# Kernel optimization log

Hardware: AMD Instinct MI355X
Metric: run time of the kernel (lower is better)

## Reference

```python
import jax, jax.numpy as jnp
import numpy as np

B, C, H, W, K = 4, 64, 128, 128, 3
K2 = K * K
PAD = (K - 1) // 2  # same padding for 3x3


def setup_inputs() -> dict:
    key = jax.random.key(0)
    ks = jax.random.split(key, 9)
    s = 0.05
    return {
        "x": jax.random.normal(ks[0], (B, C, H, W), jnp.float32),
        "inter": jax.random.normal(ks[1], (B, C, H, W), jnp.float32),
        # offset/mask predictor conv: input cat([x, inter]) -> 3*K2 channels (dy, dx, mask)
        "w_offset": jax.random.normal(ks[2], (3 * K2, 2 * C, K, K), jnp.float32) * s,
        "b_offset": jnp.zeros((3 * K2,), jnp.float32),
        # deformable conv weight (bias=False per DGM init)
        "w_dcn": jax.random.normal(ks[3], (C, C, K, K), jnp.float32) * s,
        # SFT gamma branch: two 1x1 convs (bias=False)
        "w_g1": jax.random.normal(ks[4], (C, C), jnp.float32) * s,
        "w_g2": jax.random.normal(ks[5], (C, C), jnp.float32) * s,
        # SFT beta branch: two 1x1 convs (bias=False)
        "w_b1": jax.random.normal(ks[6], (C, C), jnp.float32) * s,
        "w_b2": jax.random.normal(ks[7], (C, C), jnp.float32) * s,
    }


def _lrelu(v):
    # LeakyReLU(0.1)
    return jnp.where(v >= 0, v, 0.1 * v)


def _conv(x, w, b=None):
    y = jax.lax.conv_general_dilated(
        x, w, window_strides=(1, 1), padding=[(PAD, PAD), (PAD, PAD)],
        dimension_numbers=("NCHW", "OIHW", "NCHW"))
    if b is not None:
        y = y + b[None, :, None, None]
    return y


def _bilinear_gather(x, py, px):
    """x: [B,C,H,W]; py, px: [B,K2,H,W] float sample coords.
    Returns samples [B,K2,H,W,C]; out-of-bounds treated as zero (DCN zero-pad)."""
    y0 = jnp.floor(py)
    x0 = jnp.floor(px)
    wy = (py - y0)[..., None]
    wx = (px - x0)[..., None]

    def gather(yi, xi):
        valid = ((yi >= 0) & (yi < H) & (xi >= 0) & (xi < W)).astype(x.dtype)
        yc = jnp.clip(yi, 0, H - 1).astype(jnp.int32)
        xc = jnp.clip(xi, 0, W - 1).astype(jnp.int32)
        bidx = jnp.arange(B)[:, None, None, None]
        v = x[bidx, :, yc, xc]  # advanced indexing -> [B,K2,H,W,C]
        return v * valid[..., None]

    v00 = gather(y0, x0)
    v01 = gather(y0, x0 + 1)
    v10 = gather(y0 + 1, x0)
    v11 = gather(y0 + 1, x0 + 1)
    return (v00 * (1 - wy) * (1 - wx) + v01 * (1 - wy) * wx
            + v10 * wy * (1 - wx) + v11 * wy * wx)


def _dgm_forward(x, inter, w_offset, b_offset, w_dcn, w_g1, w_g2, w_b1, w_b2):
    # --- WADCN branch: modulated deformable conv, offsets predicted from cat(x, inter)
    om = _conv(jnp.concatenate([x, inter], axis=1), w_offset, b_offset)  # [B,3K2,H,W]
    dy, dx, m = jnp.split(om, 3, axis=1)  # each [B,K2,H,W]
    mask = jax.nn.sigmoid(m)

    ky, kx = jnp.meshgrid(jnp.arange(K), jnp.arange(K), indexing="ij")
    ky = ky.reshape(K2).astype(x.dtype)
    kx = kx.reshape(K2).astype(x.dtype)
    hh = jnp.arange(H, dtype=x.dtype)
    ww = jnp.arange(W, dtype=x.dtype)
    # sample coords: base grid + kernel-tap offset + learned offset
    py = hh[None, None, :, None] + (ky - PAD)[None, :, None, None] + dy  # [B,K2,H,W]
    px = ww[None, None, None, :] + (kx - PAD)[None, :, None, None] + dx

    samp = _bilinear_gather(x, py, px) * mask[..., None]  # [B,K2,H,W,C]
    dcn_out = jnp.einsum("bkhwc,ock->bohw", samp, w_dcn.reshape(C, C, K2))

    # --- SFT branch: two 1x1-conv + LeakyReLU chains producing gamma/beta
    gamma = jnp.einsum("oc,bchw->bohw", w_g2,
                       _lrelu(jnp.einsum("oc,bchw->bohw", w_g1, inter)))
    beta = jnp.einsum("oc,bchw->bohw", w_b2,
                      _lrelu(jnp.einsum("oc,bchw->bohw", w_b1, inter)))
    sft_out = x * gamma + beta

    # --- fused residual combine (DGM.relu is defined but never applied)
    return x + dcn_out + sft_out


def reference(x, inter, w_offset, b_offset, w_dcn, w_g1, w_g2, w_b1, w_b2):
    return _dgm_forward(x, inter, w_offset, b_offset, w_dcn, w_g1, w_g2, w_b1, w_b2)
```

## Files before the change

kernel.cpp:

```cpp
#include <hip/hip_runtime.h>
#include <hip/hip_bf16.h>
#include <math.h>

#define BB 4
#define CC 64
#define HH 128
#define WW 128
#define HW (HH*WW)
#define NPIX (BB*HW)

typedef __attribute__((ext_vector_type(8))) short short8;
typedef __attribute__((ext_vector_type(4))) float f32x4;

__device__ __forceinline__ float bf2f(ushort u) {
  union { unsigned u; float f; } v; v.u = ((unsigned)u) << 16; return v.f;
}
__device__ __forceinline__ ushort f2bf(float f) {
  __hip_bfloat16 h = __float2bfloat16(f); return *(ushort*)&h;
}

__global__ __launch_bounds__(256) void k_transp(
    const float* __restrict__ x, const float* __restrict__ inter,
    ushort* __restrict__ x_clh, ushort* __restrict__ inter_clh) {
  __shared__ float tile[64 * 129];
  int blk = blockIdx.x;
  int sel = blk >> 9;
  int bh = blk & 511;
  int b = bh >> 7, h = bh & 127;
  const float* src = sel ? inter : x;
  ushort* dst = sel ? inter_clh : x_clh;
  const float* sp = src + (size_t)(b * 64) * HW + h * WW;
  for (int i = threadIdx.x; i < 64 * 128; i += 256) {
    int c = i >> 7, w = i & 127;
    tile[c * 129 + w] = sp[(size_t)c * HW + w];
  }
  __syncthreads();
  ushort* dp = dst + ((size_t)b * HW + h * WW) * 64;
  for (int i = threadIdx.x; i < 64 * 128; i += 256) {
    int w = i >> 6, c = i & 63;
    dp[w * 64 + c] = f2bf(tile[c * 129 + w]);
  }
}

__global__ void k_wprep(const float* __restrict__ w_off,
                        const float* __restrict__ w_dcn,
                        const float* __restrict__ wg1, const float* __restrict__ wb1,
                        const float* __restrict__ wg2, const float* __restrict__ wb2,
                        ushort* __restrict__ wfb, ushort* __restrict__ wdT,
                        ushort* __restrict__ w1gb, ushort* __restrict__ w1bb,
                        ushort* __restrict__ w2gb, ushort* __restrict__ w2bb,
                        float* __restrict__ zp) {
  int blk = blockIdx.x;
  if (blk < 144) {
    int i = blk * 256 + threadIdx.x;
    if (i < 64) zp[i] = 0.f;
    if (i < 9 * 32 * 128) {
      int tap = i >> 12, rem = i & 4095, m = rem >> 7, c = rem & 127;
      float v = (m < 27) ? w_off[(size_t)(m * 128 + c) * 9 + tap] : 0.f;
      wfb[i] = f2bf(v);
    }
  } else if (blk < 288) {
    int i = (blk - 144) * 256 + threadIdx.x;
    if (i < 64 * 64 * 9) {
      int o = i / 576, rem = i % 576, k = rem >> 6, c = rem & 63;
      wdT[i] = f2bf(w_dcn[(o * 64 + c) * 9 + k]);
    }
  } else {
    int i = (blk - 288) * 256 + threadIdx.x;
    int m = i >> 12, j = i & 4095;
    const float* src = (m == 0) ? wg1 : (m == 1) ? wb1 : (m == 2) ? wg2 : wb2;
    ushort* dst = (m == 0) ? w1gb : (m == 1) ? w1bb : (m == 2) ? w2gb : w2bb;
    dst[j] = f2bf(src[j]);
  }
}

#define FPITCH 72

__global__ __launch_bounds__(256) void k_sft(
    const float* __restrict__ x, const ushort* __restrict__ inter_clh,
    const ushort* __restrict__ w1gb, const ushort* __restrict__ w1bb,
    const ushort* __restrict__ w2gb, const ushort* __restrict__ w2bb,
    float* __restrict__ out) {
  __shared__ ushort Sg[64 * FPITCH];
  __shared__ ushort Sb[64 * FPITCH];
  int tid = threadIdx.x;
  int lane = tid & 63;
  int quad = lane >> 4, col = lane & 15;
  int pg0 = blockIdx.x * 64;
  int b = pg0 >> 14, hw0 = pg0 & 16383;
  int o_base = __builtin_amdgcn_readfirstlane((tid >> 6) * 16);

  f32x4 ag[4], ab[4];
#pragma unroll
  for (int nt = 0; nt < 4; ++nt) {
    ag[nt] = (f32x4){0.f, 0.f, 0.f, 0.f};
    ab[nt] = (f32x4){0.f, 0.f, 0.f, 0.f};
  }
#pragma unroll
  for (int ks = 0; ks < 2; ++ks) {
    short8 a_g = *(const short8*)(w1gb + (size_t)(o_base + col) * 64 + ks * 32 + quad * 8);
    short8 a_b = *(const short8*)(w1bb + (size_t)(o_base + col) * 64 + ks * 32 + quad * 8);
#pragma unroll
    for (int nt = 0; nt < 4; ++nt) {
      short8 bf = *(const short8*)(inter_clh + (size_t)(pg0 + nt * 16 + col) * 64 + ks * 32 + quad * 8);
      ag[nt] = __builtin_amdgcn_mfma_f32_16x16x32_bf16(a_g, bf, ag[nt], 0, 0, 0);
      ab[nt] = __builtin_amdgcn_mfma_f32_16x16x32_bf16(a_b, bf, ab[nt], 0, 0, 0);
    }
  }
#pragma unroll
  for (int nt = 0; nt < 4; ++nt) {
    int px = nt * 16 + col;
    ushort pkg[4], pkb[4];
#pragma unroll
    for (int r = 0; r < 4; ++r) {
      float vg = ag[nt][r]; vg = vg >= 0.f ? vg : 0.1f * vg;
      float vb = ab[nt][r]; vb = vb >= 0.f ? vb : 0.1f * vb;
      pkg[r] = f2bf(vg); pkb[r] = f2bf(vb);
    }
    *(uint2*)(&Sg[px * FPITCH + o_base + quad * 4]) = *(uint2*)pkg;
    *(uint2*)(&Sb[px * FPITCH + o_base + quad * 4]) = *(uint2*)pkb;
  }
  __syncthreads();

  f32x4 gg[4], gb[4];
#pragma unroll
  for (int nt = 0; nt < 4; ++nt) {
    gg[nt] = (f32x4){0.f, 0.f, 0.f, 0.f};
    gb[nt] = (f32x4){0.f, 0.f, 0.f, 0.f};
  }
#pragma unroll
  for (int ks = 0; ks < 2; ++ks) {
    short8 a_g = *(const short8*)(w2gb + (size_t)(o_base + col) * 64 + ks * 32 + quad * 8);
    short8 a_b = *(const short8*)(w2bb + (size_t)(o_base + col) * 64 + ks * 32 + quad * 8);
#pragma unroll
    for (int nt = 0; nt < 4; ++nt) {
      short8 bg = *(const short8*)(Sg + (nt * 16 + col) * FPITCH + ks * 32 + quad * 8);
      short8 bb = *(const short8*)(Sb + (nt * 16 + col) * FPITCH + ks * 32 + quad * 8);
      gg[nt] = __builtin_amdgcn_mfma_f32_16x16x32_bf16(a_g, bg, gg[nt], 0, 0, 0);
      gb[nt] = __builtin_amdgcn_mfma_f32_16x16x32_bf16(a_b, bb, gb[nt], 0, 0, 0);
    }
  }

#pragma unroll
  for (int nt = 0; nt < 4; ++nt) {
#pragma unroll
    for (int r = 0; r < 4; ++r) {
      int o = o_base + quad * 4 + r;
      size_t idx = (size_t)(b * 64 + o) * HW + hw0 + nt * 16 + col;
      float xv = x[idx];
      out[idx] = xv + xv * gg[nt][r] + gb[nt][r];
    }
  }
}

__global__ __launch_bounds__(256) void k_convm(
    const ushort* __restrict__ x_clh, const ushort* __restrict__ inter_clh,
    const ushort* __restrict__ wfb, const ushort* __restrict__ zp,
    float* __restrict__ om) {
  int tid = threadIdx.x;
  int wave = tid >> 6, lane = tid & 63;
  int quad = lane >> 4, col = lane & 15;
  int blk = blockIdx.x;
  int b = blk >> 8, h = (blk >> 1) & 127, half = blk & 1;
  int px = half * 64 + wave * 16 + col;

  f32x4 acc0 = {0.f, 0.f, 0.f, 0.f}, acc1 = {0.f, 0.f, 0.f, 0.f};

  const ushort* src0 = x_clh + (size_t)b * HW * 64;
  const ushort* src1 = inter_clh + (size_t)b * HW * 64;

#pragma unroll
  for (int ky = 0; ky < 3; ++ky) {
    int hs = h + ky - 1;
    bool hok = (unsigned)hs < 128u;
#pragma unroll
    for (int kx = 0; kx < 3; ++kx) {
      int tap = ky * 3 + kx;
      int ps = px + kx - 1;
      bool ok = hok && ((unsigned)ps < 128u);
      int pofs = ((hs << 7) + ps) * 64 + quad * 8;
      const ushort* wbase = wfb + (size_t)tap * 4096 + (size_t)col * 128 + quad * 8;
#pragma unroll
      for (int g = 0; g < 2; ++g) {
        const ushort* sb = g ? src1 : src0;
#pragma unroll
        for (int ks = 0; ks < 2; ++ks) {
          const ushort* bp = ok ? (sb + pofs + ks * 32) : zp;
          short8 bfr = *(const short8*)bp;
          short8 a0 = *(const short8*)(wbase + g * 64 + ks * 32);
          short8 a1 = *(const short8*)(wbase + 16 * 128 + g * 64 + ks * 32);
          acc0 = __builtin_amdgcn_mfma_f32_16x16x32_bf16(a0, bfr, acc0, 0, 0, 0);
          acc1 = __builtin_amdgcn_mfma_f32_16x16x32_bf16(a1, bfr, acc1, 0, 0, 0);
        }
      }
    }
  }

  int pg = b * HW + h * WW + px;
#pragma unroll
  for (int r = 0; r < 4; ++r) {
    int o0 = quad * 4 + r;
    om[(size_t)o0 * NPIX + pg] = acc0[r];
    int o1 = 16 + quad * 4 + r;
    if (o1 < 27) om[(size_t)o1 * NPIX + pg] = acc1[r];
  }
}

#define SPITCH 200
#define NPX 32

__global__ __launch_bounds__(256) void k_dcn(
    const ushort* __restrict__ x_clh, const float* __restrict__ om,
    const float* __restrict__ b_off, const ushort* __restrict__ wdT,
    const ushort* __restrict__ zp16,
    float* __restrict__ out) {
  __shared__ ushort S[NPX * SPITCH];
  __shared__ int   cy[9 * NPX], cx[9 * NPX];
  __shared__ float cwy[9 * NPX], cwx[9 * NPX], cm[9 * NPX];

  int tid = threadIdx.x;
  int wave = tid >> 6, lane = tid & 63;
  int quad = lane >> 4, col = lane & 15;
  int rr = lane >> 3, g = lane & 7;
  int pg0 = blockIdx.x * NPX;
  int b = pg0 >> 14;
  int o_base = __builtin_amdgcn_readfirstlane(wave * 16);

  for (int i = tid; i < 9 * NPX; i += 256) {
    int k = i >> 5, p = i & 31;
    int pg = pg0 + p;
    int hw = pg & 16383;
    int h = hw >> 7, w = hw & 127;
    float dy = om[(size_t)k * NPIX + pg] + b_off[k];
    float dx = om[(size_t)(9 + k) * NPIX + pg] + b_off[9 + k];
    float mz = om[(size_t)(18 + k) * NPIX + pg] + b_off[18 + k];
    float py = (float)(h + (k / 3) - 1) + dy;
    float px = (float)(w + (k % 3) - 1) + dx;
    float y0f = floorf(py), x0f = floorf(px);
    cy[i] = (int)y0f;
    cx[i] = (int)x0f;
    cwy[i] = py - y0f;
    cwx[i] = px - x0f;
    cm[i] = 1.f / (1.f + __expf(-mz));
  }

  f32x4 acc[2];
  acc[0] = (f32x4){0.f, 0.f, 0.f, 0.f};
  acc[1] = (f32x4){0.f, 0.f, 0.f, 0.f};

  const ushort* bp = x_clh + (size_t)b * HW * 64;

  for (int chunk = 0; chunk < 3; ++chunk) {
    __syncthreads();
#pragma unroll
    for (int it = 0; it < 3; ++it) {
      int p = wave * 8 + rr;
      int idx = (chunk * 3 + it) * NPX + p;
      int y0 = cy[idx], x0 = cx[idx];
      float wy = cwy[idx], wx = cwx[idx], m = cm[idx];
      bool yok0 = (unsigned)y0 < 128u, yok1 = (unsigned)(y0 + 1) < 128u;
      bool xok0 = (unsigned)x0 < 128u, xok1 = (unsigned)(x0 + 1) < 128u;
      const ushort* r0 = bp + ((size_t)(int)((y0 << 7) + x0)) * 64 + g * 8;
      const ushort* r1 = r0 + (size_t)WW * 64;
      short8 s00 = *(const short8*)((yok0 && xok0) ? r0 : zp16);
      short8 s01 = *(const short8*)((yok0 && xok1) ? (r0 + 64) : zp16);
      short8 s10 = *(const short8*)((yok1 && xok0) ? r1 : zp16);
      short8 s11 = *(const short8*)((yok1 && xok1) ? (r1 + 64) : zp16);
      short8 outv;
#pragma unroll
      for (int j = 0; j < 8; ++j) {
        float v00 = bf2f((ushort)s00[j]), v01 = bf2f((ushort)s01[j]);
        float v10 = bf2f((ushort)s10[j]), v11 = bf2f((ushort)s11[j]);
        float top = v00 + (v01 - v00) * wx;
        float bot = v10 + (v11 - v10) * wx;
        float val = top + (bot - top) * wy;
        outv[j] = (short)f2bf(val * m);
      }
      *(short8*)(&S[p * SPITCH + it * 64 + g * 8]) = outv;
    }
    __syncthreads();
    const ushort* wrow = wdT + (size_t)(o_base + col) * 576 + chunk * 192 + quad * 8;
    const ushort* srow = S + quad * 8;
#pragma unroll
    for (int ks = 0; ks < 6; ++ks) {
      short8 a = *(const short8*)(wrow + ks * 32);
#pragma unroll
      for (int nt = 0; nt < 2; ++nt) {
        short8 bf = *(const short8*)(srow + (nt * 16 + col) * SPITCH + ks * 32);
        acc[nt] = __builtin_amdgcn_mfma_f32_16x16x32_bf16(a, bf, acc[nt], 0, 0, 0);
      }
    }
  }

  int hw0 = pg0 & 16383;
#pragma unroll
  for (int nt = 0; nt < 2; ++nt) {
#pragma unroll
    for (int r = 0; r < 4; ++r) {
      int o = o_base + quad * 4 + r;
      size_t idx = (size_t)(b * 64 + o) * HW + hw0 + nt * 16 + col;
      out[idx] += acc[nt][r];
    }
  }
}

extern "C" void kernel_launch(void* const* d_in, const int* in_sizes, int n_in,
                              void* d_out, int out_size, void* d_ws, size_t ws_size,
                              hipStream_t stream) {
  const float* x     = (const float*)d_in[0];
  const float* inter = (const float*)d_in[1];
  const float* w_off = (const float*)d_in[2];
  const float* b_off = (const float*)d_in[3];
  const float* w_dcn = (const float*)d_in[4];
  const float* wg1   = (const float*)d_in[5];
  const float* wg2   = (const float*)d_in[6];
  const float* wb1   = (const float*)d_in[7];
  const float* wb2   = (const float*)d_in[8];
  float* out = (float*)d_out;

  float* ws        = (float*)d_ws;
  ushort* x_clh    = (ushort*)ws;
  ushort* inter_clh= (ushort*)(ws + 2097152);
  float* om        = ws + 4194304;
  ushort* wfb      = (ushort*)(ws + 5963776);
  ushort* wdT      = (ushort*)(ws + 5982208);
  ushort* w1gb     = (ushort*)(ws + 6000640);
  ushort* w1bb     = (ushort*)(ws + 6002688);
  ushort* w2gb     = (ushort*)(ws + 6004736);
  ushort* w2bb     = (ushort*)(ws + 6006784);
  float* zp        = ws + 6008832;

  k_transp<<<1024, 256, 0, stream>>>(x, inter, x_clh, inter_clh);
  k_wprep<<<352, 256, 0, stream>>>(w_off, w_dcn, wg1, wb1, wg2, wb2,
                                   wfb, wdT, w1gb, w1bb, w2gb, w2bb, zp);

  k_sft<<<1024, 256, 0, stream>>>(x, inter_clh, w1gb, w1bb, w2gb, w2bb, out);

  k_convm<<<1024, 256, 0, stream>>>(x_clh, inter_clh, wfb, (const ushort*)zp, om);

  k_dcn<<<2048, 256, 0, stream>>>(x_clh, om, b_off, wdT, (const ushort*)zp, out);
}
```

Before: 191.3 us.

## Hoist offset-conv weights into registers and split output channels across waves

```diff
diff --git a/kernel.cpp b/kernel.cpp
--- a/kernel.cpp
+++ b/kernel.cpp
@@ -18,6 +18,10 @@
 __device__ __forceinline__ ushort f2bf(float f) {
   __hip_bfloat16 h = __float2bfloat16(f); return *(ushort*)&h;
 }
+
+#define XOFS   0u
+#define IOFS   4194304u
+#define ZPOFS  12017664u
 
 __global__ __launch_bounds__(256) void k_transp(
     const float* __restrict__ x, const float* __restrict__ inter,
@@ -153,56 +157,68 @@
   }
 }
 
-__global__ __launch_bounds__(256) void k_convm(
-    const ushort* __restrict__ x_clh, const ushort* __restrict__ inter_clh,
-    const ushort* __restrict__ wfb, const ushort* __restrict__ zp,
+__global__ __launch_bounds__(256, 2) void k_convm(
+    const ushort* __restrict__ wsb, const ushort* __restrict__ wfb,
     float* __restrict__ om) {
   int tid = threadIdx.x;
   int wave = tid >> 6, lane = tid & 63;
   int quad = lane >> 4, col = lane & 15;
   int blk = blockIdx.x;
-  int b = blk >> 8, h = (blk >> 1) & 127, half = blk & 1;
-  int px = half * 64 + wave * 16 + col;
-
-  f32x4 acc0 = {0.f, 0.f, 0.f, 0.f}, acc1 = {0.f, 0.f, 0.f, 0.f};
-
-  const ushort* src0 = x_clh + (size_t)b * HW * 64;
-  const ushort* src1 = inter_clh + (size_t)b * HW * 64;
-
-#pragma unroll
-  for (int ky = 0; ky < 3; ++ky) {
-    int hs = h + ky - 1;
-    bool hok = (unsigned)hs < 128u;
-#pragma unroll
-    for (int kx = 0; kx < 3; ++kx) {
-      int tap = ky * 3 + kx;
-      int ps = px + kx - 1;
-      bool ok = hok && ((unsigned)ps < 128u);
-      int pofs = ((hs << 7) + ps) * 64 + quad * 8;
-      const ushort* wbase = wfb + (size_t)tap * 4096 + (size_t)col * 128 + quad * 8;
-#pragma unroll
-      for (int g = 0; g < 2; ++g) {
-        const ushort* sb = g ? src1 : src0;
-#pragma unroll
-        for (int ks = 0; ks < 2; ++ks) {
-          const ushort* bp = ok ? (sb + pofs + ks * 32) : zp;
-          short8 bfr = *(const short8*)bp;
-          short8 a0 = *(const short8*)(wbase + g * 64 + ks * 32);
-          short8 a1 = *(const short8*)(wbase + 16 * 128 + g * 64 + ks * 32);
-          acc0 = __builtin_amdgcn_mfma_f32_16x16x32_bf16(a0, bfr, acc0, 0, 0, 0);
-          acc1 = __builtin_amdgcn_mfma_f32_16x16x32_bf16(a1, bfr, acc1, 0, 0, 0);
-        }
+  int b = blk >> 7, h = blk & 127;
+  int half = wave >> 1, mt = wave & 1;
+
+  short8 A[36];
+  {
+    const ushort* wb0 = wfb + (size_t)(mt * 16 + col) * 128 + quad * 8;
+#pragma unroll
+    for (int tap = 0; tap < 9; ++tap)
+#pragma unroll
+      for (int g = 0; g < 2; ++g)
+#pragma unroll
+        for (int ks = 0; ks < 2; ++ks)
+          A[tap * 4 + g * 2 + ks] =
+              *(const short8*)(wb0 + (size_t)tap * 4096 + g * 64 + ks * 32);
+  }
+
+  unsigned bslab = (unsigned)b * HW * 64;
+  int pgrow = b * HW + h * WW;
+
+#pragma unroll 1
+  for (int t = 0; t < 4; ++t) {
+    int px = half * 64 + t * 16 + col;
+    unsigned ofs[9];
+#pragma unroll
+    for (int ky = 0; ky < 3; ++ky) {
+      int hs = h + ky - 1;
+      bool hok = (unsigned)hs < 128u;
+#pragma unroll
+      for (int kx = 0; kx < 3; ++kx) {
+        int ps = px + kx - 1;
+        bool ok = hok && ((unsigned)ps < 128u);
+        unsigned o = bslab + (unsigned)((hs << 7) + ps) * 64 + quad * 8;
+        ofs[ky * 3 + kx] = ok ? o : ZPOFS;
       }
     }
-  }
-
-  int pg = b * HW + h * WW + px;
-#pragma unroll
-  for (int r = 0; r < 4; ++r) {
-    int o0 = quad * 4 + r;
-    om[(size_t)o0 * NPIX + pg] = acc0[r];
-    int o1 = 16 + quad * 4 + r;
-    if (o1 < 27) om[(size_t)o1 * NPIX + pg] = acc1[r];
+    f32x4 accx = {0.f, 0.f, 0.f, 0.f}, acci = {0.f, 0.f, 0.f, 0.f};
+#pragma unroll
+    for (int tap = 0; tap < 9; ++tap) {
+      const ushort* p = wsb + ofs[tap];
+      short8 bx0 = *(const short8*)(p + XOFS);
+      short8 bx1 = *(const short8*)(p + XOFS + 32);
+      short8 bi0 = *(const short8*)(p + IOFS);
+      short8 bi1 = *(const short8*)(p + IOFS + 32);
+      accx = __builtin_amdgcn_mfma_f32_16x16x32_bf16(A[tap * 4 + 0], bx0, accx, 0, 0, 0);
+      accx = __builtin_amdgcn_mfma_f32_16x16x32_bf16(A[tap * 4 + 1], bx1, accx, 0, 0, 0);
+      acci = __builtin_amdgcn_mfma_f32_16x16x32_bf16(A[tap * 4 + 2], bi0, acci, 0, 0, 0);
+      acci = __builtin_amdgcn_mfma_f32_16x16x32_bf16(A[tap * 4 + 3], bi1, acci, 0, 0, 0);
+    }
+    int pg = pgrow + px;
+#pragma unroll
+    for (int r = 0; r < 4; ++r) {
+      int o = mt * 16 + quad * 4 + r;
+      float v = accx[r] + acci[r];
+      if (o < 27) om[(size_t)o * NPIX + pg] = v;
+    }
   }
 }
 
@@ -319,6 +335,7 @@
   float* out = (float*)d_out;
 
   float* ws        = (float*)d_ws;
+  ushort* wsb      = (ushort*)d_ws;
   ushort* x_clh    = (ushort*)ws;
   ushort* inter_clh= (ushort*)(ws + 2097152);
   float* om        = ws + 4194304;
@@ -336,7 +353,7 @@
 
   k_sft<<<1024, 256, 0, stream>>>(x, inter_clh, w1gb, w1bb, w2gb, w2bb, out);
 
-  k_convm<<<1024, 256, 0, stream>>>(x_clh, inter_clh, wfb, (const ushort*)zp, om);
+  k_convm<<<512, 256, 0, stream>>>(wsb, wfb, om);
 
   k_dcn<<<2048, 256, 0, stream>>>(x_clh, om, b_off, wdT, (const ushort*)zp, out);
 }
```

Result: faster. 183.7 us (-4.0%).

## Stage 3x3 conv input halo tile in LDS and split output channels across waves

Applied to the files above, without the earlier changes.

```diff
diff --git a/kernel.cpp b/kernel.cpp
--- a/kernel.cpp
+++ b/kernel.cpp
@@ -153,56 +153,71 @@
   }
 }
 
+#define CPITCH 72
+
 __global__ __launch_bounds__(256) void k_convm(
     const ushort* __restrict__ x_clh, const ushort* __restrict__ inter_clh,
-    const ushort* __restrict__ wfb, const ushort* __restrict__ zp,
-    float* __restrict__ om) {
+    const ushort* __restrict__ wfb, float* __restrict__ om) {
+  __shared__ ushort S[6 * 34 * CPITCH];
   int tid = threadIdx.x;
   int wave = tid >> 6, lane = tid & 63;
   int quad = lane >> 4, col = lane & 15;
   int blk = blockIdx.x;
-  int b = blk >> 8, h = (blk >> 1) & 127, half = blk & 1;
-  int px = half * 64 + wave * 16 + col;
-
-  f32x4 acc0 = {0.f, 0.f, 0.f, 0.f}, acc1 = {0.f, 0.f, 0.f, 0.f};
-
-  const ushort* src0 = x_clh + (size_t)b * HW * 64;
-  const ushort* src1 = inter_clh + (size_t)b * HW * 64;
+  int b = blk >> 9, h = (blk >> 2) & 127, wq = blk & 3;
+  int pt = wave >> 1, mt = wave & 1;
+
+  {
+    int ch = (tid & 7) * 8;
+    unsigned bbase = (unsigned)b * HW;
+#pragma unroll
+    for (int it = 0; it < 7; ++it) {
+      int e = it * 32 + (tid >> 3);
+      if (e < 204) {
+        int srcrow = e / 34, pxl = e % 34;
+        int src = srcrow / 3, row = srcrow % 3;
+        int hs = h + row - 1;
+        int ps = wq * 32 + pxl - 1;
+        bool ok = ((unsigned)hs < 128u) && ((unsigned)ps < 128u);
+        int hc = hs < 0 ? 0 : (hs > 127 ? 127 : hs);
+        int pc = ps < 0 ? 0 : (ps > 127 ? 127 : ps);
+        const ushort* sb = src ? inter_clh : x_clh;
+        short8 v = *(const short8*)(sb + ((size_t)(bbase + (hc << 7) + pc)) * 64 + ch);
+        short8 z = {0, 0, 0, 0, 0, 0, 0, 0};
+        if (!ok) v = z;
+        *(short8*)(&S[e * CPITCH + ch]) = v;
+      }
+    }
+  }
+  __syncthreads();
+
+  f32x4 accx = {0.f, 0.f, 0.f, 0.f}, acci = {0.f, 0.f, 0.f, 0.f};
+  const ushort* wb0 = wfb + (size_t)(mt * 16 + col) * 128 + quad * 8;
+  int pxb = pt * 16 + col;
 
 #pragma unroll
   for (int ky = 0; ky < 3; ++ky) {
-    int hs = h + ky - 1;
-    bool hok = (unsigned)hs < 128u;
 #pragma unroll
     for (int kx = 0; kx < 3; ++kx) {
       int tap = ky * 3 + kx;
-      int ps = px + kx - 1;
-      bool ok = hok && ((unsigned)ps < 128u);
-      int pofs = ((hs << 7) + ps) * 64 + quad * 8;
-      const ushort* wbase = wfb + (size_t)tap * 4096 + (size_t)col * 128 + quad * 8;
-#pragma unroll
-      for (int g = 0; g < 2; ++g) {
-        const ushort* sb = g ? src1 : src0;
-#pragma unroll
-        for (int ks = 0; ks < 2; ++ks) {
-          const ushort* bp = ok ? (sb + pofs + ks * 32) : zp;
-          short8 bfr = *(const short8*)bp;
-          short8 a0 = *(const short8*)(wbase + g * 64 + ks * 32);
-          short8 a1 = *(const short8*)(wbase + 16 * 128 + g * 64 + ks * 32);
-          acc0 = __builtin_amdgcn_mfma_f32_16x16x32_bf16(a0, bfr, acc0, 0, 0, 0);
-          acc1 = __builtin_amdgcn_mfma_f32_16x16x32_bf16(a1, bfr, acc1, 0, 0, 0);
-        }
+      const ushort* wt = wb0 + (size_t)tap * 4096;
+#pragma unroll
+      for (int ks = 0; ks < 2; ++ks) {
+        short8 a0 = *(const short8*)(wt + ks * 32);
+        short8 b0 = *(const short8*)(&S[(ky * 34 + pxb + kx) * CPITCH + ks * 32 + quad * 8]);
+        accx = __builtin_amdgcn_mfma_f32_16x16x32_bf16(a0, b0, accx, 0, 0, 0);
+        short8 a1 = *(const short8*)(wt + 64 + ks * 32);
+        short8 b1 = *(const short8*)(&S[((3 + ky) * 34 + pxb + kx) * CPITCH + ks * 32 + quad * 8]);
+        acci = __builtin_amdgcn_mfma_f32_16x16x32_bf16(a1, b1, acci, 0, 0, 0);
       }
     }
   }
 
-  int pg = b * HW + h * WW + px;
+  int pg = b * HW + h * WW + wq * 32 + pt * 16 + col;
 #pragma unroll
   for (int r = 0; r < 4; ++r) {
-    int o0 = quad * 4 + r;
-    om[(size_t)o0 * NPIX + pg] = acc0[r];
-    int o1 = 16 + quad * 4 + r;
-    if (o1 < 27) om[(size_t)o1 * NPIX + pg] = acc1[r];
+    int o = mt * 16 + quad * 4 + r;
+    float v = accx[r] + acci[r];
+    if (o < 27) om[(size_t)o * NPIX + pg] = v;
   }
 }
 
@@ -336,7 +351,7 @@
 
   k_sft<<<1024, 256, 0, stream>>>(x, inter_clh, w1gb, w1bb, w2gb, w2bb, out);
 
-  k_convm<<<1024, 256, 0, stream>>>(x_clh, inter_clh, wfb, (const ushort*)zp, om);
+  k_convm<<<2048, 256, 0, stream>>>(x_clh, inter_clh, wfb, om);
 
   k_dcn<<<2048, 256, 0, stream>>>(x_clh, om, b_off, wdT, (const ushort*)zp, out);
 }
```

After: 181.1 us. 1.06x faster.
